# Performance work log

Measured on AMD Instinct MI355X. Metric: run time of the kernel, lower is better.

The kernel has to match this reference:

```python
import jax, jax.numpy as jnp
import numpy as np

B, N, C = 4, 1024, 1024
H = 16
D = C // H  # 64
HID = int(int(C * 4.0) * 2 / 3)  # 2730
EPS = 1e-6


def rmsnorm(x, w):
    return x * jax.lax.rsqrt(jnp.mean(x * x, axis=-1, keepdims=True) + EPS) * w


def rope_cos_sin(n, d):
    inv_freq = 1.0 / (10000.0 ** (jnp.arange(0, d, 2, dtype=jnp.float32) / d))
    t = jnp.arange(n, dtype=jnp.float32)
    freqs = jnp.einsum('i,j->ij', t, inv_freq)  # [N, D/2]
    emb = jnp.concatenate([freqs, freqs], axis=-1)  # [N, D]
    return jnp.cos(emb), jnp.sin(emb)


def rotate_half(x):
    x1, x2 = jnp.split(x, 2, axis=-1)
    return jnp.concatenate([-x2, x1], axis=-1)


def setup_inputs() -> dict:
    key = jax.random.key(0)
    ks = jax.random.split(key, 12)
    s = lambda fan_in: 1.0 / np.sqrt(fan_in)
    return {
        'x': jax.random.normal(ks[0], (B, N, C), jnp.float32),
        'c': jax.random.normal(ks[1], (B, C), jnp.float32),
        'norm1_w': jnp.ones((C,), jnp.float32),
        'norm2_w': jnp.ones((C,), jnp.float32),
        'qkv_w': jax.random.normal(ks[2], (C, 3 * C), jnp.float32) * s(C),
        'proj_w': jax.random.normal(ks[3], (C, C), jnp.float32) * s(C),
        'proj_b': jnp.zeros((C,), jnp.float32),
        'qn_w': jnp.ones((D,), jnp.float32),
        'kn_w': jnp.ones((D,), jnp.float32),
        'w1': jax.random.normal(ks[4], (C, HID), jnp.float32) * s(C),
        'w2': jax.random.normal(ks[5], (HID, C), jnp.float32) * s(HID),
        'w3': jax.random.normal(ks[6], (C, HID), jnp.float32) * s(C),
        'ada_w': jax.random.normal(ks[7], (C, 6 * C), jnp.float32) * s(C),
        'ada_b': jnp.zeros((6 * C,), jnp.float32),
    }


def reference(x, c, norm1_w, norm2_w, qkv_w, proj_w, proj_b, qn_w, kn_w, w1, w2, w3, ada_w, ada_b):
    # AdaLN modulation params from conditioning
    mods = jax.nn.silu(c) @ ada_w + ada_b  # [B, 6C]
    sh_msa, sc_msa, g_msa, sh_mlp, sc_mlp, g_mlp = jnp.split(mods, 6, axis=-1)

    # --- attention branch ---
    x_mod = rmsnorm(x, norm1_w) * (1 + sc_msa[:, None, :]) + sh_msa[:, None, :]
    qkv = (x_mod @ qkv_w).reshape(B, N, 3, H, D).transpose(2, 0, 3, 1, 4)  # [3,B,H,N,D]
    q, k, v = qkv[0], qkv[1], qkv[2]
    q = rmsnorm(q, qn_w)
    k = rmsnorm(k, kn_w)
    cos, sin = rope_cos_sin(N, D)  # [N, D]
    q = q * cos + rotate_half(q) * sin
    k = k * cos + rotate_half(k) * sin
    attn = jax.nn.softmax(jnp.einsum('bhqd,bhkd->bhqk', q, k) * (D ** -0.5), axis=-1)
    o = jnp.einsum('bhqk,bhkd->bhqd', attn, v).transpose(0, 2, 1, 3).reshape(B, N, C)
    x = x + g_msa[:, None, :] * (o @ proj_w + proj_b)

    # --- SwiGLU MLP branch ---
    x_mod = rmsnorm(x, norm2_w) * (1 + sc_mlp[:, None, :]) + sh_mlp[:, None, :]
    mlp = (jax.nn.silu(x_mod @ w1) * (x_mod @ w3)) @ w2
    x = x + g_mlp[:, None, :] * mlp
    return x
```

## Files before the change

### kernel.cpp

```cpp
#include <hip/hip_runtime.h>
#include <hip/hip_bf16.h>
#include <stdint.h>

using bf16 = __hip_bfloat16;
using bf16x8 = __attribute__((ext_vector_type(8))) short;
using f32x4  = __attribute__((ext_vector_type(4))) float;
using short4v = __attribute__((ext_vector_type(4))) short;

#define EPSF 1e-6f

__device__ __forceinline__ unsigned short f2bu(float x) {
  union { bf16 h; unsigned short u; } cvt;
  cvt.h = __float2bfloat16(x);
  return cvt.u;
}

typedef __attribute__((address_space(3))) void as3_void;
typedef const __attribute__((address_space(1))) void as1_void;

__device__ __forceinline__ void gload_lds16(const void* g, void* l) {
  as1_void* gp = (as1_void*)(uintptr_t)g;
  as3_void* lp = (as3_void*)(uint32_t)(uintptr_t)l;
  __builtin_amdgcn_global_load_lds(gp, lp, 16, 0, 0);
}

__global__ void rope_tab(float* __restrict__ cosT, float* __restrict__ sinT) {
  const int i = blockIdx.x * 256 + threadIdx.x;
  const int n = i >> 5, fi = i & 31;
  const float invf = powf(10000.f, -(float)fi * (1.f / 32.f));
  const float ang = (float)n * invf;
  cosT[i] = cosf(ang);
  sinT[i] = sinf(ang);
}

__global__ void __launch_bounds__(256) ada_part(const float* __restrict__ cc,
                                                const float* __restrict__ adaw,
                                                float* __restrict__ part) {
  __shared__ float sc[256];
  __shared__ float red[1024];
  const int t = threadIdx.x;
  const int cb = blockIdx.x % 48, ks = blockIdx.x / 48;
  const int k0 = ks * 64;
  {
    const int b = t >> 6, kk = t & 63;
    const float v = cc[b * 1024 + k0 + kk];
    sc[t] = v / (1.f + __expf(-v));
  }
  __syncthreads();
  const int colL = t & 127, kh = t >> 7;
  const int col = cb * 128 + colL;
  float a0 = 0.f, a1 = 0.f, a2 = 0.f, a3 = 0.f;
  const float* ap = adaw + (size_t)(k0 + kh * 32) * 6144 + col;
#pragma unroll
  for (int k = 0; k < 32; ++k) {
    const float awv = ap[(size_t)k * 6144];
    const int kk = kh * 32 + k;
    a0 += sc[kk] * awv; a1 += sc[64 + kk] * awv;
    a2 += sc[128 + kk] * awv; a3 += sc[192 + kk] * awv;
  }
  red[kh * 512 + 0 * 128 + colL] = a0;
  red[kh * 512 + 1 * 128 + colL] = a1;
  red[kh * 512 + 2 * 128 + colL] = a2;
  red[kh * 512 + 3 * 128 + colL] = a3;
  __syncthreads();
  if (kh == 0) {
#pragma unroll
    for (int b = 0; b < 4; ++b) {
      const float s = red[b * 128 + colL] + red[512 + b * 128 + colL];
      part[(size_t)(ks * 4 + b) * 6144 + col] = s;
    }
  }
}

__global__ void __launch_bounds__(256) ada_reduce(const float* __restrict__ part,
                                                  const float* __restrict__ adab,
                                                  float* __restrict__ mods) {
  const int i = blockIdx.x * 256 + threadIdx.x;
  const int b = i / 6144, col = i % 6144;
  float s = adab[col];
#pragma unroll
  for (int ks = 0; ks < 16; ++ks) s += part[(size_t)(ks * 4 + b) * 6144 + col];
  mods[b * 6144 + col] = s;
}

__global__ void __launch_bounds__(256) norm_mod(const float* __restrict__ X,
                                                const float* __restrict__ wgt,
                                                const float* __restrict__ mods,
                                                int sh_off, int sc_off,
                                                bf16* __restrict__ Y) {
  __shared__ float red[4];
  const int row = blockIdx.x, t = threadIdx.x, l = t & 63, wv = t >> 6;
  const float4 xv = ((const float4*)(X + (size_t)row * 1024))[t];
  float ss = xv.x * xv.x + xv.y * xv.y + xv.z * xv.z + xv.w * xv.w;
#pragma unroll
  for (int off = 1; off < 64; off <<= 1) ss += __shfl_xor(ss, off);
  if (l == 0) red[wv] = ss;
  __syncthreads();
  ss = (red[0] + red[1]) + (red[2] + red[3]);
  const float rs = rsqrtf(ss * (1.f / 1024.f) + EPSF);
  const int b = row >> 10;
  const float* mb = mods + b * 6144;
  const int c0 = t * 4;
  float vals[4] = {xv.x, xv.y, xv.z, xv.w};
  short4v yv;
#pragma unroll
  for (int j = 0; j < 4; j++) {
    const int cc = c0 + j;
    const float y = vals[j] * rs * wgt[cc] * (1.f + mb[sc_off + cc]) + mb[sh_off + cc];
    yv[j] = (short)f2bu(y);
  }
  *(short4v*)(Y + (size_t)row * 1024 + c0) = yv;
}

__global__ void __launch_bounds__(256) transpose_cast(const float* __restrict__ src, int R, int Cc,
                                                      bf16* __restrict__ dst, int ldd) {
  __shared__ float tile[32][33];
  const int tx = threadIdx.x & 31, ty = threadIdx.x >> 5;
  const int ct = blockIdx.x * 32, rt = blockIdx.y * 32;
#pragma unroll
  for (int kk = 0; kk < 4; ++kk) {
    const int r = rt + ty + kk * 8;
    float v = 0.f;
    if (r < R && (ct + tx) < Cc) v = src[(size_t)r * Cc + ct + tx];
    tile[ty + kk * 8][tx] = v;
  }
  __syncthreads();
#pragma unroll
  for (int kk = 0; kk < 4; ++kk) {
    const int c = ct + ty + kk * 8;
    const int r = rt + tx;
    if (c < Cc && r < ldd) dst[(size_t)c * ldd + r] = __float2bfloat16(tile[tx][ty + kk * 8]);
  }
}

template <int TN, int EPI>
__global__ void __launch_bounds__(256, 3) gemm_p(const bf16* __restrict__ A, int lda,
                                                 const bf16* __restrict__ Bt, int ldb,
                                                 int K, int Nreal, int ldc, int nx,
                                                 bf16* __restrict__ outb,
                                                 float* __restrict__ outf,
                                                 const float* __restrict__ resid,
                                                 const float* __restrict__ gate,
                                                 const float* __restrict__ bias) {
  constexpr int BUFSZ = 8192 + TN * 64;
  constexpr int WN = (TN == 128) ? 2 : 1;
  constexpr int MI = (TN == 128) ? 4 : 2;
  constexpr int WTM = (TN == 128) ? 64 : 32;
  __shared__ char smB[3 * BUFSZ];
  const int t = threadIdx.x, l = t & 63, w = t >> 6;
  const int g = l >> 4, cl = l & 15;
  const int cpx = gridDim.x >> 3;
  const int wg = blockIdx.x;
  const int swz0 = (wg & 7) * cpx + (wg >> 3);
  const int m0 = (swz0 / nx) * 128, n0 = (swz0 % nx) * TN;
  const int wm = w / WN, wn = w % WN;
  f32x4 acc[MI][4] = {};
  const int NK = K >> 5;
  const int srow = t >> 2;
  const int scol = (((t & 3) ^ ((t >> 3) & 3))) * 8;
  const int rsw = (cl >> 1) & 3;

  auto stage = [&](int kt, int buf) {
    char* dst = smB + buf * BUFSZ;
    const int kk = kt * 32 + scol;
    gload_lds16(A + (size_t)(m0 + srow) * lda + kk,      dst + t * 16);
    gload_lds16(A + (size_t)(m0 + 64 + srow) * lda + kk, dst + 4096 + t * 16);
    gload_lds16(Bt + (size_t)(n0 + srow) * ldb + kk,     dst + 8192 + t * 16);
    if constexpr (TN == 128)
      gload_lds16(Bt + (size_t)(n0 + 64 + srow) * ldb + kk, dst + 12288 + t * 16);
  };

  stage(0, 0);
  stage(1, 1);
  if constexpr (TN == 128) asm volatile("s_waitcnt vmcnt(4)" ::: "memory");
  else                     asm volatile("s_waitcnt vmcnt(3)" ::: "memory");
  __builtin_amdgcn_s_barrier();
  __builtin_amdgcn_sched_barrier(0);
  int cur = 0;
  for (int kt = 0; kt < NK; ++kt) {
    if (kt + 2 < NK) stage(kt + 2, (cur >= 1) ? cur - 1 : 2);
    const bf16* Ab = (const bf16*)(smB + cur * BUFSZ);
    const bf16* Bb = (const bf16*)(smB + cur * BUFSZ + 8192);
    bf16x8 af[MI], bfr[4];
#pragma unroll
    for (int i = 0; i < MI; i++)
      af[i] = *(const bf16x8*)&Ab[(wm * WTM + i * 16 + cl) * 32 + ((g ^ rsw) << 3)];
#pragma unroll
    for (int i = 0; i < 4; i++)
      bfr[i] = *(const bf16x8*)&Bb[(wn * 64 + i * 16 + cl) * 32 + ((g ^ rsw) << 3)];
    __builtin_amdgcn_s_setprio(1);
#pragma unroll
    for (int mi = 0; mi < MI; mi++)
#pragma unroll
      for (int ni = 0; ni < 4; ni++)
        acc[mi][ni] = __builtin_amdgcn_mfma_f32_16x16x32_bf16(af[mi], bfr[ni], acc[mi][ni], 0, 0, 0);
    __builtin_amdgcn_s_setprio(0);
    if (kt + 2 < NK) {
      if constexpr (TN == 128) asm volatile("s_waitcnt vmcnt(4)" ::: "memory");
      else                     asm volatile("s_waitcnt vmcnt(3)" ::: "memory");
    } else {
      asm volatile("s_waitcnt vmcnt(0)" ::: "memory");
    }
    __builtin_amdgcn_s_barrier();
    __builtin_amdgcn_sched_barrier(0);
    cur = (cur + 1 == 3) ? 0 : cur + 1;
  }
#pragma unroll
  for (int mi = 0; mi < MI; mi++) {
#pragma unroll
    for (int ni = 0; ni < 4; ni++) {
      const int c = n0 + wn * 64 + ni * 16 + cl;
#pragma unroll
      for (int j = 0; j < 4; j++) {
        const int r = m0 + wm * WTM + mi * 16 + g * 4 + j;
        const float v = acc[mi][ni][j];
        if constexpr (EPI == 0) {
          if (c < Nreal) outb[(size_t)r * ldc + c] = __float2bfloat16(v);
        } else if constexpr (EPI == 1) {
          const int b = r >> 10;
          outf[(size_t)r * ldc + c] = resid[(size_t)r * ldc + c] + gate[b * 6144 + c] * (v + bias[c]);
        } else if constexpr (EPI == 4) {
          const int b = r >> 10;
          outf[(size_t)r * ldc + c] = resid[(size_t)r * ldc + c] + gate[b * 6144 + c] * v;
        }
      }
    }
  }
}

__global__ void __launch_bounds__(256, 2) gemm_w13(const bf16* __restrict__ A, int lda,
                                                   const bf16* __restrict__ B1t,
                                                   const bf16* __restrict__ B3t, int ldb,
                                                   int K, int Nreal, int ldc, int nx,
                                                   bf16* __restrict__ outb) {
  constexpr int BUFSZ = 24576;
  __shared__ char smB[3 * BUFSZ];
  const int t = threadIdx.x, l = t & 63, w = t >> 6;
  const int g = l >> 4, cl = l & 15;
  const int cpx = gridDim.x >> 3;
  const int wg = blockIdx.x;
  const int swz0 = (wg & 7) * cpx + (wg >> 3);
  const int m0 = (swz0 / nx) * 128, n0 = (swz0 % nx) * 128;
  const int wm = w >> 1, wn = w & 1;
  f32x4 acc1[4][4] = {}, acc3[4][4] = {};
  const int NK = K >> 5;
  const int srow = t >> 2;
  const int scol = (((t & 3) ^ ((t >> 3) & 3))) * 8;
  const int rsw = (cl >> 1) & 3;

  auto stage = [&](int kt, int buf) {
    char* dst = smB + buf * BUFSZ;
    const int kk = kt * 32 + scol;
    gload_lds16(A   + (size_t)(m0 + srow) * lda + kk,      dst + t * 16);
    gload_lds16(A   + (size_t)(m0 + 64 + srow) * lda + kk, dst + 4096 + t * 16);
    gload_lds16(B1t + (size_t)(n0 + srow) * ldb + kk,      dst + 8192 + t * 16);
    gload_lds16(B1t + (size_t)(n0 + 64 + srow) * ldb + kk, dst + 12288 + t * 16);
    gload_lds16(B3t + (size_t)(n0 + srow) * ldb + kk,      dst + 16384 + t * 16);
    gload_lds16(B3t + (size_t)(n0 + 64 + srow) * ldb + kk, dst + 20480 + t * 16);
  };

  stage(0, 0);
  stage(1, 1);
  asm volatile("s_waitcnt vmcnt(6)" ::: "memory");
  __builtin_amdgcn_s_barrier();
  __builtin_amdgcn_sched_barrier(0);
  int cur = 0;
  for (int kt = 0; kt < NK; ++kt) {
    if (kt + 2 < NK) stage(kt + 2, (cur >= 1) ? cur - 1 : 2);
    const bf16* Ab  = (const bf16*)(smB + cur * BUFSZ);
    const bf16* B1b = (const bf16*)(smB + cur * BUFSZ + 8192);
    const bf16* B3b = (const bf16*)(smB + cur * BUFSZ + 16384);
    bf16x8 af[4], b1r[4], b3r[4];
#pragma unroll
    for (int i = 0; i < 4; i++)
      af[i] = *(const bf16x8*)&Ab[(wm * 64 + i * 16 + cl) * 32 + ((g ^ rsw) << 3)];
#pragma unroll
    for (int i = 0; i < 4; i++) {
      b1r[i] = *(const bf16x8*)&B1b[(wn * 64 + i * 16 + cl) * 32 + ((g ^ rsw) << 3)];
      b3r[i] = *(const bf16x8*)&B3b[(wn * 64 + i * 16 + cl) * 32 + ((g ^ rsw) << 3)];
    }
    __builtin_amdgcn_s_setprio(1);
#pragma unroll
    for (int mi = 0; mi < 4; mi++)
#pragma unroll
      for (int ni = 0; ni < 4; ni++) {
        acc1[mi][ni] = __builtin_amdgcn_mfma_f32_16x16x32_bf16(af[mi], b1r[ni], acc1[mi][ni], 0, 0, 0);
        acc3[mi][ni] = __builtin_amdgcn_mfma_f32_16x16x32_bf16(af[mi], b3r[ni], acc3[mi][ni], 0, 0, 0);
      }
    __builtin_amdgcn_s_setprio(0);
    if (kt + 2 < NK) asm volatile("s_waitcnt vmcnt(6)" ::: "memory");
    else             asm volatile("s_waitcnt vmcnt(0)" ::: "memory");
    __builtin_amdgcn_s_barrier();
    __builtin_amdgcn_sched_barrier(0);
    cur = (cur + 1 == 3) ? 0 : cur + 1;
  }
#pragma unroll
  for (int mi = 0; mi < 4; mi++) {
#pragma unroll
    for (int ni = 0; ni < 4; ni++) {
      const int c = n0 + wn * 64 + ni * 16 + cl;
#pragma unroll
      for (int j = 0; j < 4; j++) {
        const int r = m0 + wm * 64 + mi * 16 + g * 4 + j;
        if (c < Nreal) {
          const float hv = acc1[mi][ni][j];
          const float sl = hv / (1.f + __expf(-hv));
          outb[(size_t)r * ldc + c] = __float2bfloat16(sl * acc3[mi][ni][j]);
        } else {
          outb[(size_t)r * ldc + c] = __float2bfloat16(0.f);
        }
      }
    }
  }
}

__global__ void __launch_bounds__(256) qkv_post(const bf16* __restrict__ qkv,
                                                const float* __restrict__ cosT,
                                                const float* __restrict__ sinT,
                                                const float* __restrict__ qnw,
                                                const float* __restrict__ knw,
                                                bf16* __restrict__ Qo, bf16* __restrict__ Ko) {
  const int t = threadIdx.x, l = t & 63, wv = t >> 6;
  const int row = blockIdx.x * 4 + wv;
  const int token = row >> 4, h = row & 15;
  const int b = token >> 10, n = token & 1023;
  const int d = l;
  const bf16* base = qkv + (size_t)token * 3072 + h * 64 + d;
  float q = __bfloat162float(base[0]);
  float k = __bfloat162float(base[1024]);
  float sq = q * q, sk = k * k;
#pragma unroll
  for (int off = 1; off < 64; off <<= 1) {
    sq += __shfl_xor(sq, off);
    sk += __shfl_xor(sk, off);
  }
  q *= rsqrtf(sq * (1.f / 64.f) + EPSF) * qnw[d];
  k *= rsqrtf(sk * (1.f / 64.f) + EPSF) * knw[d];
  const float cs = cosT[n * 32 + (d & 31)];
  const float sn = sinT[n * 32 + (d & 31)];
  const float qx = __shfl_xor(q, 32), kx = __shfl_xor(k, 32);
  const float sgn = (d < 32) ? -1.f : 1.f;
  const float qo = (q * cs + sgn * qx * sn) * 0.125f;
  const float ko = k * cs + sgn * kx * sn;
  const size_t ob = ((size_t)(b * 16 + h) * 1024 + n) * 64 + d;
  Qo[ob] = __float2bfloat16(qo);
  Ko[ob] = __float2bfloat16(ko);
}

__global__ void __launch_bounds__(256) vtrans(const bf16* __restrict__ qkv,
                                              bf16* __restrict__ vbt) {
  __shared__ unsigned short tile[64 * 64];
  const int t = threadIdx.x;
  const int bh = blockIdx.y, nt = blockIdx.x;
  const int b = bh >> 4, h = bh & 15;
  const int n0 = nt * 64;
#pragma unroll
  for (int rep = 0; rep < 2; ++rep) {
    const int ci = t + rep * 256;
    const int r = ci >> 3, dc = ci & 7;
    const bf16x8 v = *(const bf16x8*)(qkv + (size_t)(b * 1024 + n0 + r) * 3072 + 2048 + h * 64 + dc * 8);
#pragma unroll
    for (int j = 0; j < 8; ++j) {
      const int d = dc * 8 + j;
      const int chunk = (r >> 3) ^ (d & 7) ^ ((d >> 3) & 7);
      tile[d * 64 + chunk * 8 + (r & 7)] = (unsigned short)v[j];
    }
  }
  __syncthreads();
#pragma unroll
  for (int rep = 0; rep < 2; ++rep) {
    const int ci = t + rep * 256;
    const int d = ci >> 3, nc = ci & 7;
    const int phys = nc ^ (d & 7) ^ ((d >> 3) & 7);
    const bf16x8 v = *(const bf16x8*)&tile[d * 64 + phys * 8];
    *(bf16x8*)(vbt + (size_t)bh * 65536 + (size_t)d * 1024 + n0 + nc * 8) = v;
  }
}

__global__ void __launch_bounds__(256) attn_fwd(const bf16* __restrict__ Qb,
                                                const bf16* __restrict__ Kb,
                                                const bf16* __restrict__ Vb,
                                                bf16* __restrict__ Ob) {
  __shared__ char KsB[2 * 8192];
  __shared__ char VsB[2 * 8192];
  __shared__ unsigned short Ps[4 * 16 * 64];
  const int t = threadIdx.x, l = t & 63, w = t >> 6;
  const int g = l >> 4, cl = l & 15;
  const int bh = blockIdx.y;
  const int q0 = blockIdx.x * 64;
  const bf16* Qg = Qb + (size_t)bh * 65536;
  const bf16* Kg = Kb + (size_t)bh * 65536;
  const bf16* Vg = Vb + (size_t)bh * 65536;
  const int qrow = q0 + w * 16 + cl;
  const bf16x8 aq0 = *(const bf16x8*)(Qg + (size_t)qrow * 64 + g * 8);
  const bf16x8 aq1 = *(const bf16x8*)(Qg + (size_t)qrow * 64 + 32 + g * 8);
  float mreg = -1e30f, lreg = 0.f;
  f32x4 o[4] = {};
  const int kr_l = w * 8 + (l >> 3);
  const int ku = (l & 7) ^ (l >> 3);
  unsigned short* Pw = Ps + w * 1024;
  const int sxor = cl & 7;

  auto stageKV = [&](int kvt, int buf) {
    const int kv0 = kvt * 64;
    char* kd = KsB + buf * 8192 + w * 1024;
    char* vd = VsB + buf * 8192 + w * 1024;
    gload_lds16(Kg + (size_t)(kv0 + kr_l) * 64 + ku * 8, kd);
    gload_lds16(Kg + (size_t)(kv0 + 32 + kr_l) * 64 + ku * 8, kd + 4096);
    gload_lds16(Vg + (size_t)kr_l * 1024 + kv0 + ku * 8, vd);
    gload_lds16(Vg + (size_t)(kr_l + 32) * 1024 + kv0 + ku * 8, vd + 4096);
  };

  stageKV(0, 0);
  for (int kvt = 0; kvt < 16; ++kvt) {
    const int cb = kvt & 1;
    if (kvt + 1 < 16) {
      stageKV(kvt + 1, cb ^ 1);
      asm volatile("s_waitcnt vmcnt(4)" ::: "memory");
    } else {
      asm volatile("s_waitcnt vmcnt(0)" ::: "memory");
    }
    __builtin_amdgcn_s_barrier();
    __builtin_amdgcn_sched_barrier(0);
    const char* Kt = KsB + cb * 8192;
    const char* Vt = VsB + cb * 8192;
    f32x4 s[4] = {};
#pragma unroll
    for (int ch = 0; ch < 4; ch++) {
      const int rb = (16 * ch + cl) << 7;
      const bf16x8 bk0 = *(const bf16x8*)(Kt + rb + ((g ^ sxor) << 4));
      s[ch] = __builtin_amdgcn_mfma_f32_16x16x32_bf16(bk0, aq0, s[ch], 0, 0, 0);
      const bf16x8 bk1 = *(const bf16x8*)(Kt + rb + (((4 + g) ^ sxor) << 4));
      s[ch] = __builtin_amdgcn_mfma_f32_16x16x32_bf16(bk1, aq1, s[ch], 0, 0, 0);
    }
    float pm = fmaxf(fmaxf(fmaxf(s[0][0], s[0][1]), fmaxf(s[0][2], s[0][3])),
                     fmaxf(fmaxf(s[1][0], s[1][1]), fmaxf(s[1][2], s[1][3])));
    pm = fmaxf(pm, fmaxf(fmaxf(fmaxf(s[2][0], s[2][1]), fmaxf(s[2][2], s[2][3])),
                         fmaxf(fmaxf(s[3][0], s[3][1]), fmaxf(s[3][2], s[3][3]))));
    pm = fmaxf(pm, __shfl_xor(pm, 16));
    pm = fmaxf(pm, __shfl_xor(pm, 32));
    const float nm = fmaxf(mreg, pm);
    const float al = __expf(mreg - nm);
    mreg = nm;
    float rs = 0.f;
#pragma unroll
    for (int ch = 0; ch < 4; ch++) {
      const float p0 = __expf(s[ch][0] - nm);
      const float p1 = __expf(s[ch][1] - nm);
      const float p2 = __expf(s[ch][2] - nm);
      const float p3 = __expf(s[ch][3] - nm);
      rs += (p0 + p1) + (p2 + p3);
      short4v pk;
      pk[0] = (short)f2bu(p0); pk[1] = (short)f2bu(p1);
      pk[2] = (short)f2bu(p2); pk[3] = (short)f2bu(p3);
      const int phys = (2 * ch + (g >> 1)) ^ sxor;
      *(short4v*)&Pw[cl * 64 + phys * 8 + 4 * (g & 1)] = pk;
    }
    rs += __shfl_xor(rs, 16);
    rs += __shfl_xor(rs, 32);
    lreg = lreg * al + rs;
#pragma unroll
    for (int dc = 0; dc < 4; dc++) {
      o[dc][0] *= al; o[dc][1] *= al; o[dc][2] *= al; o[dc][3] *= al;
    }
    const bf16x8 pa0 = *(const bf16x8*)&Pw[cl * 64 + ((g ^ sxor) << 3)];
    const bf16x8 pa1 = *(const bf16x8*)&Pw[cl * 64 + (((4 + g) ^ sxor) << 3)];
#pragma unroll
    for (int dc = 0; dc < 4; dc++) {
      const int vr = (16 * dc + cl) << 7;
      const bf16x8 bv0 = *(const bf16x8*)(Vt + vr + ((g ^ sxor) << 4));
      o[dc] = __builtin_amdgcn_mfma_f32_16x16x32_bf16(bv0, pa0, o[dc], 0, 0, 0);
      const bf16x8 bv1 = *(const bf16x8*)(Vt + vr + (((4 + g) ^ sxor) << 4));
      o[dc] = __builtin_amdgcn_mfma_f32_16x16x32_bf16(bv1, pa1, o[dc], 0, 0, 0);
    }
    __builtin_amdgcn_s_barrier();
  }
  const int b = bh >> 4, h = bh & 15;
  const float inv = 1.f / lreg;
  const int q = q0 + w * 16 + cl;
  const size_t base = ((size_t)(b * 1024 + q) * 16 + h) * 64;
#pragma unroll
  for (int dc = 0; dc < 4; dc++) {
    short4v ov;
    ov[0] = (short)f2bu(o[dc][0] * inv);
    ov[1] = (short)f2bu(o[dc][1] * inv);
    ov[2] = (short)f2bu(o[dc][2] * inv);
    ov[3] = (short)f2bu(o[dc][3] * inv);
    *(short4v*)(Ob + base + 16 * dc + 4 * g) = ov;
  }
}

extern "C" void kernel_launch(void* const* d_in, const int* in_sizes, int n_in,
                              void* d_out, int out_size, void* d_ws, size_t ws_size,
                              hipStream_t stream) {
  const float* x     = (const float*)d_in[0];
  const float* c     = (const float*)d_in[1];
  const float* n1w   = (const float*)d_in[2];
  const float* n2w   = (const float*)d_in[3];
  const float* qkvw  = (const float*)d_in[4];
  const float* projw = (const float*)d_in[5];
  const float* projb = (const float*)d_in[6];
  const float* qnw   = (const float*)d_in[7];
  const float* knw   = (const float*)d_in[8];
  const float* w1    = (const float*)d_in[9];
  const float* w2    = (const float*)d_in[10];
  const float* w3    = (const float*)d_in[11];
  const float* adaw  = (const float*)d_in[12];
  const float* adab  = (const float*)d_in[13];
  float* outp = (float*)d_out;
  char* ws = (char*)d_ws;
  if (ws_size < 93159424u) return;

  float* ropeC = (float*)(ws + 0);
  float* ropeS = (float*)(ws + 131072);
  float* mods  = (float*)(ws + 262144);
  bf16* xmod   = (bf16*)(ws + 360448);
  bf16* qkvwt  = (bf16*)(ws + 8749056);
  bf16* projwt = (bf16*)(ws + 15040512);
  bf16* w1t    = (bf16*)(ws + 17137664);
  bf16* w3t    = (bf16*)(ws + 22904832);
  bf16* w2t    = (bf16*)(ws + 28672000);
  bf16* qkv    = (bf16*)(ws + 34439168);
  float* apart = (float*)(ws + 34439168);
  bf16* qb     = (bf16*)(ws + 59604992);
  bf16* gbuf   = (bf16*)(ws + 59604992);
  bf16* kb     = (bf16*)(ws + 67993600);
  bf16* vbt    = (bf16*)(ws + 76382208);
  bf16* ob     = (bf16*)(ws + 84770816);

  rope_tab<<<128, 256, 0, stream>>>(ropeC, ropeS);
  ada_part<<<768, 256, 0, stream>>>(c, adaw, apart);
  ada_reduce<<<96, 256, 0, stream>>>(apart, adab, mods);
  transpose_cast<<<dim3(96, 32), 256, 0, stream>>>(qkvw, 1024, 3072, qkvwt, 1024);
  transpose_cast<<<dim3(32, 32), 256, 0, stream>>>(projw, 1024, 1024, projwt, 1024);
  transpose_cast<<<dim3(86, 32), 256, 0, stream>>>(w1, 1024, 2730, w1t, 1024);
  transpose_cast<<<dim3(86, 32), 256, 0, stream>>>(w3, 1024, 2730, w3t, 1024);
  transpose_cast<<<dim3(32, 88), 256, 0, stream>>>(w2, 2730, 1024, w2t, 2816);

  norm_mod<<<4096, 256, 0, stream>>>(x, n1w, mods, 0, 1024, xmod);
  gemm_p<128, 0><<<768, 256, 0, stream>>>(xmod, 1024, qkvwt, 1024, 1024, 3072, 3072, 24,
                                          qkv, nullptr, nullptr, nullptr, nullptr);
  vtrans<<<dim3(16, 64), 256, 0, stream>>>(qkv, vbt);
  qkv_post<<<16384, 256, 0, stream>>>(qkv, ropeC, ropeS, qnw, knw, qb, kb);
  attn_fwd<<<dim3(16, 64), 256, 0, stream>>>(qb, kb, vbt, ob);
  gemm_p<64, 1><<<512, 256, 0, stream>>>(ob, 1024, projwt, 1024, 1024, 1024, 1024, 16,
                                         nullptr, outp, x, mods + 2048, projb);

  norm_mod<<<4096, 256, 0, stream>>>(outp, n2w, mods, 3072, 4096, xmod);
  gemm_w13<<<704, 256, 0, stream>>>(xmod, 1024, w1t, w3t, 1024, 1024, 2730, 2816, 22,
                                    gbuf);
  gemm_p<64, 4><<<512, 256, 0, stream>>>(gbuf, 2816, w2t, 2816, 2816, 1024, 1024, 16,
                                         nullptr, outp, outp, mods + 5120, nullptr);
}
```

Baseline: 266.3 us.

## Use dual-B GEMM for QKV and widen attention blocks to 8 waves

The QKV projection now runs on the dual-B GEMM kernel. Each block computes two adjacent 128-column tiles (128x256) from one shared A tile, which halves A reloads and the block count. The attention kernel moves to 512-thread blocks covering 128 query rows per (batch, head), so each K/V tile staged in LDS serves twice as many queries, and staging is spread across all eight waves. The trade-offs are higher register pressure in the larger blocks and fewer blocks in flight.

```diff
diff --git a/kernel.cpp b/kernel.cpp
--- a/kernel.cpp
+++ b/kernel.cpp
@@ -228,19 +228,21 @@
   }
 }
 
-__global__ void __launch_bounds__(256, 2) gemm_w13(const bf16* __restrict__ A, int lda,
-                                                   const bf16* __restrict__ B1t,
-                                                   const bf16* __restrict__ B3t, int ldb,
-                                                   int K, int Nreal, int ldc, int nx,
-                                                   bf16* __restrict__ outb) {
+template <int EPI>
+__global__ void __launch_bounds__(256, 2) gemm_dual(const bf16* __restrict__ A, int lda,
+                                                    const bf16* __restrict__ B1t,
+                                                    const bf16* __restrict__ B3t, int ldb,
+                                                    int K, int Nreal, int ldc, int nx,
+                                                    bf16* __restrict__ outb) {
   constexpr int BUFSZ = 24576;
+  constexpr int NSTEP = (EPI == 0) ? 256 : 128;
   __shared__ char smB[3 * BUFSZ];
   const int t = threadIdx.x, l = t & 63, w = t >> 6;
   const int g = l >> 4, cl = l & 15;
   const int cpx = gridDim.x >> 3;
   const int wg = blockIdx.x;
   const int swz0 = (wg & 7) * cpx + (wg >> 3);
-  const int m0 = (swz0 / nx) * 128, n0 = (swz0 % nx) * 128;
+  const int m0 = (swz0 / nx) * 128, n0 = (swz0 % nx) * NSTEP;
   const int wm = w >> 1, wn = w & 1;
   f32x4 acc1[4][4] = {}, acc3[4][4] = {};
   const int NK = K >> 5;
@@ -302,12 +304,17 @@
 #pragma unroll
       for (int j = 0; j < 4; j++) {
         const int r = m0 + wm * 64 + mi * 16 + g * 4 + j;
-        if (c < Nreal) {
-          const float hv = acc1[mi][ni][j];
-          const float sl = hv / (1.f + __expf(-hv));
-          outb[(size_t)r * ldc + c] = __float2bfloat16(sl * acc3[mi][ni][j]);
+        if constexpr (EPI == 0) {
+          outb[(size_t)r * ldc + c] = __float2bfloat16(acc1[mi][ni][j]);
+          outb[(size_t)r * ldc + c + 128] = __float2bfloat16(acc3[mi][ni][j]);
         } else {
-          outb[(size_t)r * ldc + c] = __float2bfloat16(0.f);
+          if (c < Nreal) {
+            const float hv = acc1[mi][ni][j];
+            const float sl = hv / (1.f + __expf(-hv));
+            outb[(size_t)r * ldc + c] = __float2bfloat16(sl * acc3[mi][ni][j]);
+          } else {
+            outb[(size_t)r * ldc + c] = __float2bfloat16(0.f);
+          }
         }
       }
     }
@@ -377,17 +384,18 @@
   }
 }
 
-__global__ void __launch_bounds__(256) attn_fwd(const bf16* __restrict__ Qb,
+__global__ void __launch_bounds__(512) attn_fwd(const bf16* __restrict__ Qb,
                                                 const bf16* __restrict__ Kb,
                                                 const bf16* __restrict__ Vb,
                                                 bf16* __restrict__ Ob) {
   __shared__ char KsB[2 * 8192];
   __shared__ char VsB[2 * 8192];
-  __shared__ unsigned short Ps[4 * 16 * 64];
+  __shared__ unsigned short Ps[8 * 16 * 64];
   const int t = threadIdx.x, l = t & 63, w = t >> 6;
   const int g = l >> 4, cl = l & 15;
-  const int bh = blockIdx.y;
-  const int q0 = blockIdx.x * 64;
+  const int wg = blockIdx.x;
+  const int bh = wg & 63;
+  const int q0 = (wg >> 6) * 128;
   const bf16* Qg = Qb + (size_t)bh * 65536;
   const bf16* Kg = Kb + (size_t)bh * 65536;
   const bf16* Vg = Vb + (size_t)bh * 65536;
@@ -396,19 +404,15 @@
   const bf16x8 aq1 = *(const bf16x8*)(Qg + (size_t)qrow * 64 + 32 + g * 8);
   float mreg = -1e30f, lreg = 0.f;
   f32x4 o[4] = {};
-  const int kr_l = w * 8 + (l >> 3);
-  const int ku = (l & 7) ^ (l >> 3);
+  const int kr_l = t >> 3;
+  const int ku = (t & 7) ^ ((t >> 3) & 7);
   unsigned short* Pw = Ps + w * 1024;
   const int sxor = cl & 7;
 
   auto stageKV = [&](int kvt, int buf) {
     const int kv0 = kvt * 64;
-    char* kd = KsB + buf * 8192 + w * 1024;
-    char* vd = VsB + buf * 8192 + w * 1024;
-    gload_lds16(Kg + (size_t)(kv0 + kr_l) * 64 + ku * 8, kd);
-    gload_lds16(Kg + (size_t)(kv0 + 32 + kr_l) * 64 + ku * 8, kd + 4096);
-    gload_lds16(Vg + (size_t)kr_l * 1024 + kv0 + ku * 8, vd);
-    gload_lds16(Vg + (size_t)(kr_l + 32) * 1024 + kv0 + ku * 8, vd + 4096);
+    gload_lds16(Kg + (size_t)(kv0 + kr_l) * 64 + ku * 8, KsB + buf * 8192 + w * 1024);
+    gload_lds16(Vg + (size_t)kr_l * 1024 + kv0 + ku * 8, VsB + buf * 8192 + w * 1024);
   };
 
   stageKV(0, 0);
@@ -416,7 +420,7 @@
     const int cb = kvt & 1;
     if (kvt + 1 < 16) {
       stageKV(kvt + 1, cb ^ 1);
-      asm volatile("s_waitcnt vmcnt(4)" ::: "memory");
+      asm volatile("s_waitcnt vmcnt(2)" ::: "memory");
     } else {
       asm volatile("s_waitcnt vmcnt(0)" ::: "memory");
     }
@@ -538,17 +542,17 @@
   transpose_cast<<<dim3(32, 88), 256, 0, stream>>>(w2, 2730, 1024, w2t, 2816);
 
   norm_mod<<<4096, 256, 0, stream>>>(x, n1w, mods, 0, 1024, xmod);
-  gemm_p<128, 0><<<768, 256, 0, stream>>>(xmod, 1024, qkvwt, 1024, 1024, 3072, 3072, 24,
-                                          qkv, nullptr, nullptr, nullptr, nullptr);
+  gemm_dual<0><<<384, 256, 0, stream>>>(xmod, 1024, qkvwt, qkvwt + (size_t)128 * 1024, 1024,
+                                        1024, 3072, 3072, 12, qkv);
   vtrans<<<dim3(16, 64), 256, 0, stream>>>(qkv, vbt);
   qkv_post<<<16384, 256, 0, stream>>>(qkv, ropeC, ropeS, qnw, knw, qb, kb);
-  attn_fwd<<<dim3(16, 64), 256, 0, stream>>>(qb, kb, vbt, ob);
+  attn_fwd<<<512, 512, 0, stream>>>(qb, kb, vbt, ob);
   gemm_p<64, 1><<<512, 256, 0, stream>>>(ob, 1024, projwt, 1024, 1024, 1024, 1024, 16,
                                          nullptr, outp, x, mods + 2048, projb);
 
   norm_mod<<<4096, 256, 0, stream>>>(outp, n2w, mods, 3072, 4096, xmod);
-  gemm_w13<<<704, 256, 0, stream>>>(xmod, 1024, w1t, w3t, 1024, 1024, 2730, 2816, 22,
-                                    gbuf);
+  gemm_dual<3><<<704, 256, 0, stream>>>(xmod, 1024, w1t, w3t, 1024, 1024, 2730, 2816, 22,
+                                        gbuf);
   gemm_p<64, 4><<<512, 256, 0, stream>>>(gbuf, 2816, w2t, 2816, 2816, 1024, 1024, 16,
                                          nullptr, outp, outp, mods + 5120, nullptr);
 }
```

Result: faster. 259.9 us (-2.4%).
